# Kernel optimization log

Hardware: AMD Instinct MI355X
Metric: run time of the kernel (lower is better)

Reference implementation:

```python
import jax, jax.numpy as jnp
import numpy as np
import math

B, H, N, D = 4, 8, 2048, 64


def setup_inputs() -> dict:
    key = jax.random.key(0)
    kq, kk, kv = jax.random.split(key, 3)
    q = jax.random.normal(kq, (B, H, N, D), dtype=jnp.float32)
    k = jax.random.normal(kk, (B, H, N, D), dtype=jnp.float32)
    v = jax.random.normal(kv, (B, H, N, D), dtype=jnp.float32)
    return {"q": q, "k": k, "v": v}


def reference(q, k, v):
    # global_attention_Sub: expanded squared L2 distance ||q_i - k_j||^2
    # = qq_i - 2 q_i.k_j + kk_j, then softmax(-dist/sqrt(D)) @ v.
    scale = math.sqrt(q.shape[-1])
    inner = -2.0 * jnp.einsum('bhnd,bhmd->bhnm', q, k)          # [B,H,N,N]
    qq = jnp.sum(q * q, axis=-1, keepdims=True)                  # [B,H,N,1]
    kk = jnp.sum(k * k, axis=-1, keepdims=True)                  # [B,H,N,1]
    diff_sq = qq + inner + jnp.swapaxes(kk, -1, -2)              # [B,H,N,N]
    attn = jax.nn.softmax(-diff_sq / scale, axis=-1)
    x = jnp.einsum('bhnm,bhmd->bhnd', attn, v)                   # [B,H,N,D]
    return jnp.transpose(x, (0, 2, 1, 3))                        # [B,N,H,D]
```

## Files before the change

kernel.cpp:

```cpp
#include <hip/hip_runtime.h>

typedef __bf16 bf16x8 __attribute__((ext_vector_type(8)));
typedef float floatx4 __attribute__((ext_vector_type(4)));
typedef float floatx16 __attribute__((ext_vector_type(16)));
typedef unsigned int uintx4 __attribute__((ext_vector_type(4)));

constexpr int Bc = 4, Hc = 8, Nc = 2048, Dc = 64;
constexpr int BQ = 128;
constexpr int WQ = 32;
constexpr int TK = 64;
constexpr int NT = Nc / TK;
constexpr int NT2 = NT / 2;
constexpr float LOG2E = 1.44269504088896340736f;

constexpr size_t KSW_OFF = 0;
constexpr size_t VSW_OFF = (size_t)32 * NT * 8192;
constexpr size_t KKN_OFF = VSW_OFF * 2;

constexpr int SK_OFF  = 0;
constexpr int SV_OFF  = 32768;
constexpr int SKK_OFF = 65536;
constexpr int SL_OFF  = 66560;
constexpr int SMEM_BYTES = 67584;

typedef __attribute__((address_space(1))) const unsigned int gu32;
typedef __attribute__((address_space(3))) unsigned int lu32;
__device__ __forceinline__ void dma16(const void* g, void* l) {
    __builtin_amdgcn_global_load_lds((gu32*)g, (lu32*)l, 16, 0, 0);
}
__device__ __forceinline__ void dma4(const void* g, void* l) {
    __builtin_amdgcn_global_load_lds((gu32*)g, (lu32*)l, 4, 0, 0);
}

__device__ __forceinline__ unsigned pk2(float lo, float hi) {
    unsigned short a = __builtin_bit_cast(unsigned short, (__bf16)lo);
    unsigned short b = __builtin_bit_cast(unsigned short, (__bf16)hi);
    return (unsigned)a | ((unsigned)b << 16);
}

__global__ __launch_bounds__(256) void prep_kernel(
    const float* __restrict__ Kg, const float* __restrict__ Vg, char* __restrict__ ws)
{
    __shared__ float sT[64 * 68];
    const int tid = threadIdx.x;
    const int jt = blockIdx.x, bh = blockIdx.y;

    __bf16* Ksw = (__bf16*)(ws + KSW_OFF) + ((size_t)bh * NT + jt) * 4096;
    __bf16* Vsw = (__bf16*)(ws + VSW_OFF) + ((size_t)bh * NT + jt) * 4096;
    float*  kkn = (float*)(ws + KKN_OFF) + (size_t)bh * Nc + jt * 64;
    const size_t tb = ((size_t)bh * Nc + jt * 64) * Dc;

#pragma unroll
    for (int cc = 0; cc < 2; ++cc) {
        const int g   = tid + cc * 256;
        const int key = g >> 3, kcx = g & 7;
        const int kc  = kcx ^ (key & 7);
        const float* src = Kg + tb + key * 64 + kc * 8;
        float4 a = *(const float4*)src;
        float4 b = *(const float4*)(src + 4);
        float ss = a.x*a.x + a.y*a.y + a.z*a.z + a.w*a.w
                 + b.x*b.x + b.y*b.y + b.z*b.z + b.w*b.w;
        ss += __shfl_xor(ss, 1);
        ss += __shfl_xor(ss, 2);
        ss += __shfl_xor(ss, 4);
        if (kcx == 0) {
            const int k5 = key & 31, kt = key >> 5;
            const int rlo = k5 & 3, hh = (k5 >> 2) & 1, rhi = k5 >> 3;
            kkn[kt * 32 + hh * 16 + rhi * 4 + rlo] = -(ss * 0.125f * LOG2E);
        }
        bf16x8 c8;
        c8[0]=(__bf16)a.x; c8[1]=(__bf16)a.y; c8[2]=(__bf16)a.z; c8[3]=(__bf16)a.w;
        c8[4]=(__bf16)b.x; c8[5]=(__bf16)b.y; c8[6]=(__bf16)b.z; c8[7]=(__bf16)b.w;
        *(bf16x8*)(Ksw + g * 8) = c8;
    }
    {
        const int js = tid >> 2, dc = (tid & 3) * 16;
        const float* vr = Vg + tb + js * 64 + dc;
        float* dst = &sT[js * 68 + dc];
        *(float4*)dst       = *(const float4*)vr;
        *(float4*)(dst + 4) = *(const float4*)(vr + 4);
        *(float4*)(dst + 8) = *(const float4*)(vr + 8);
        *(float4*)(dst + 12)= *(const float4*)(vr + 12);
    }
    __syncthreads();
#pragma unroll
    for (int cc = 0; cc < 2; ++cc) {
        const int g = tid + cc * 256;
        const int d = g >> 3, kcx = g & 7;
        const int kc = kcx ^ (d & 7);
        bf16x8 c8;
#pragma unroll
        for (int e = 0; e < 8; ++e) {
            const int ee = (e + kcx) & 7;
            c8[ee] = (__bf16)sT[(kc * 8 + ee) * 68 + d];
        }
        *(bf16x8*)(Vsw + g * 8) = c8;
    }
}

__global__ __launch_bounds__(512, 4) void attn_kernel(
    const float* __restrict__ Qg, const char* __restrict__ ws, float* __restrict__ Og)
{
    __shared__ __align__(16) char smem[SMEM_BYTES];

    const int tid  = threadIdx.x;
    const int wave = tid >> 6;
    const int grp  = wave >> 2;
    const int sw   = wave & 3;
    const int lane = tid & 63;
    const int r31  = lane & 31;
    const int hi   = lane >> 5;

    const int lin  = blockIdx.x + (blockIdx.y << 4);
    const int xcd  = lin & 7, slot = lin >> 3;
    const int bh   = (xcd << 2) | (slot >> 4);
    const int qt   = slot & 15;

    const char* Kimg = ws + KSW_OFF + (size_t)bh * NT * 8192;
    const char* Vimg = ws + VSW_OFF + (size_t)bh * NT * 8192;
    const float* kkp = (const float*)(ws + KKN_OFF) + (size_t)bh * Nc;

    const float qscale = 0.25f * LOG2E;
    const int i0 = qt * BQ + sw * WQ;

    bf16x8 qf[4];
    {
        const float* qrow = Qg + ((size_t)bh * Nc + i0 + r31) * Dc + hi * 8;
#pragma unroll
        for (int ks = 0; ks < 4; ++ks) {
            float4 a = *(const float4*)(qrow + ks * 16);
            float4 b = *(const float4*)(qrow + ks * 16 + 4);
            bf16x8 f;
            f[0] = (__bf16)(a.x * qscale); f[1] = (__bf16)(a.y * qscale);
            f[2] = (__bf16)(a.z * qscale); f[3] = (__bf16)(a.w * qscale);
            f[4] = (__bf16)(b.x * qscale); f[5] = (__bf16)(b.y * qscale);
            f[6] = (__bf16)(b.z * qscale); f[7] = (__bf16)(b.w * qscale);
            qf[ks] = f;
        }
    }

    int off4[4];
#pragma unroll
    for (int ks = 0; ks < 4; ++ks)
        off4[ks] = r31 * 128 + (((ks * 2 + hi) ^ (r31 & 7)) << 4);

    floatx16 oacc[2];
#pragma unroll
    for (int dt = 0; dt < 2; ++dt)
#pragma unroll
        for (int e = 0; e < 16; ++e) oacc[dt][e] = 0.f;
    float lpr0 = 0.f, lpr1 = 0.f;

    auto stage = [&](int t, int nb) {
        const size_t tb = (size_t)t * 16384;
        const int off = tid * 16;
        dma16(Kimg + tb + off,        smem + SK_OFF + nb * 8192 + off);
        dma16(Kimg + tb + 8192 + off, smem + SK_OFF + 16384 + nb * 8192 + off);
        dma16(Vimg + tb + off,        smem + SV_OFF + nb * 8192 + off);
        dma16(Vimg + tb + 8192 + off, smem + SV_OFF + 16384 + nb * 8192 + off);
        if (tid < 128)
            dma4(kkp + t * 128 + tid, smem + SKK_OFF + nb * 512 + tid * 4);
    };

    stage(0, 0);

    for (int t = 0; t < NT2; ++t) {
        const int b = t & 1;
        __syncthreads();
        if (t + 1 < NT2) stage(t + 1, b ^ 1);

        const char* kb = smem + SK_OFF + grp * 16384 + b * 8192;
        const char* vb = smem + SV_OFF + grp * 16384 + b * 8192;
        const float* skkb = (const float*)(smem + SKK_OFF + b * 512) + grp * 64 + hi * 16;

        floatx16 st[2];
#pragma unroll
        for (int kt = 0; kt < 2; ++kt)
#pragma unroll
            for (int gi = 0; gi < 4; ++gi) {
                floatx4 kv = *(const floatx4*)(skkb + kt * 32 + gi * 4);
                st[kt][gi * 4 + 0] = kv[0]; st[kt][gi * 4 + 1] = kv[1];
                st[kt][gi * 4 + 2] = kv[2]; st[kt][gi * 4 + 3] = kv[3];
            }

        __builtin_amdgcn_s_setprio(1);
#pragma unroll
        for (int kt = 0; kt < 2; ++kt)
#pragma unroll
            for (int ks = 0; ks < 4; ++ks) {
                bf16x8 kf = *(const bf16x8*)(kb + kt * 4096 + off4[ks]);
                st[kt] = __builtin_amdgcn_mfma_f32_32x32x16_bf16(kf, qf[ks], st[kt], 0, 0, 0);
            }
        __builtin_amdgcn_s_setprio(0);

#pragma unroll
        for (int kt = 0; kt < 2; ++kt) {
            float p[16];
#pragma unroll
            for (int r = 0; r < 16; ++r) p[r] = __builtin_amdgcn_exp2f(st[kt][r]);
#pragma unroll
            for (int r = 0; r < 16; r += 2) { lpr0 += p[r]; lpr1 += p[r + 1]; }
            unsigned w[4][2];
#pragma unroll
            for (int g = 0; g < 4; ++g) {
                w[g][0] = pk2(p[4 * g + 0], p[4 * g + 1]);
                w[g][1] = pk2(p[4 * g + 2], p[4 * g + 3]);
            }
            __builtin_amdgcn_s_setprio(1);
#pragma unroll
            for (int sub = 0; sub < 2; ++sub) {
                unsigned a0 = w[2 * sub][0],     a1 = w[2 * sub][1];
                unsigned b0 = w[2 * sub + 1][0], b1 = w[2 * sub + 1][1];
                asm("v_permlane32_swap_b32 %0, %1" : "+v"(a0), "+v"(b0));
                asm("v_permlane32_swap_b32 %0, %1" : "+v"(a1), "+v"(b1));
                uintx4 u; u[0] = a0; u[1] = a1; u[2] = b0; u[3] = b1;
                bf16x8 pa = __builtin_bit_cast(bf16x8, u);
                const int ks = kt * 2 + sub;
#pragma unroll
                for (int dt = 0; dt < 2; ++dt) {
                    bf16x8 vf = *(const bf16x8*)(vb + dt * 4096 + off4[ks]);
                    oacc[dt] = __builtin_amdgcn_mfma_f32_32x32x16_bf16(pa, vf, oacc[dt], 0, 0, 0);
                }
            }
            __builtin_amdgcn_s_setprio(0);
        }
    }

    {
        float lpr = lpr0 + lpr1;
        float l = lpr + __shfl_xor(lpr, 32);
        if (!hi) *(float*)(smem + SL_OFF + (grp * 128 + sw * 32 + r31) * 4) = l;
    }
    __syncthreads();

    {
        char* slot = smem + wave * 4096;
        if (grp == 0) {
#pragma unroll
            for (int r = 0; r < 16; ++r)
                *(float*)(slot + r * 256 + lane * 4) = oacc[1][r];
        } else {
#pragma unroll
            for (int r = 0; r < 16; ++r)
                *(float*)(slot + r * 256 + lane * 4) = oacc[0][r];
        }
    }
    __syncthreads();

    floatx16 osum;
    if (grp == 0) osum = oacc[0]; else osum = oacc[1];
    {
        const char* pslot = smem + (wave ^ 4) * 4096;
#pragma unroll
        for (int r = 0; r < 16; ++r)
            osum[r] += *(const float*)(pslot + r * 256 + lane * 4);
    }

    const float* slp = (const float*)(smem + SL_OFF);
    const int b_ = bh >> 3, hh = bh & 7;
#pragma unroll
    for (int g = 0; g < 4; ++g) {
        floatx4 la = *(const floatx4*)(slp + sw * 32 + 8 * g + 4 * hi);
        floatx4 lb = *(const floatx4*)(slp + 128 + sw * 32 + 8 * g + 4 * hi);
#pragma unroll
        for (int rlo = 0; rlo < 4; ++rlo) {
            const float inv = 1.f / (la[rlo] + lb[rlo]);
            const int i = i0 + 8 * g + 4 * hi + rlo;
            float* orow = Og + (((size_t)b_ * Nc + i) * Hc + hh) * Dc + grp * 32 + r31;
            orow[0] = osum[4 * g + rlo] * inv;
        }
    }
}

extern "C" void kernel_launch(void* const* d_in, const int* in_sizes, int n_in,
                              void* d_out, int out_size, void* d_ws, size_t ws_size,
                              hipStream_t stream) {
    const float* q = (const float*)d_in[0];
    const float* k = (const float*)d_in[1];
    const float* v = (const float*)d_in[2];
    float* out = (float*)d_out;
    char* ws = (char*)d_ws;
    prep_kernel<<<dim3(NT, Bc * Hc), 256, 0, stream>>>(k, v, ws);
    attn_kernel<<<dim3(Nc / BQ, Bc * Hc), 512, 0, stream>>>(q, ws, out);
}
```

Measured before the change: 136.0 us.

## Software-pipeline QK^T of next tile with PV of previous tile

Restructures the main loop so each iteration issues the QK^T MFMAs for tile t together with the PV MFMAs for tile t-1, using softmax probabilities kept in registers from the previous iteration. The exp/pack softmax work then runs after the next stage's DMA is issued, so it can overlap with matrix work. A prologue and epilogue handle the first and last tiles. This adds a second __syncthreads per iteration and keeps more live registers for the pa fragments, which may hurt occupancy.

Result: no change. 138.5 us (+1.8%).

```diff
diff --git a/kernel.cpp b/kernel.cpp
--- a/kernel.cpp
+++ b/kernel.cpp
@@ -162,18 +162,8 @@
             dma4(kkp + t * 128 + tid, smem + SKK_OFF + nb * 512 + tid * 4);
     };
 
-    stage(0, 0);
-
-    for (int t = 0; t < NT2; ++t) {
-        const int b = t & 1;
-        __syncthreads();
-        if (t + 1 < NT2) stage(t + 1, b ^ 1);
-
-        const char* kb = smem + SK_OFF + grp * 16384 + b * 8192;
-        const char* vb = smem + SV_OFF + grp * 16384 + b * 8192;
+    auto kk_init = [&](int b, floatx16 st[2]) {
         const float* skkb = (const float*)(smem + SKK_OFF + b * 512) + grp * 64 + hi * 16;
-
-        floatx16 st[2];
 #pragma unroll
         for (int kt = 0; kt < 2; ++kt)
 #pragma unroll
@@ -182,17 +172,11 @@
                 st[kt][gi * 4 + 0] = kv[0]; st[kt][gi * 4 + 1] = kv[1];
                 st[kt][gi * 4 + 2] = kv[2]; st[kt][gi * 4 + 3] = kv[3];
             }
-
-        __builtin_amdgcn_s_setprio(1);
-#pragma unroll
-        for (int kt = 0; kt < 2; ++kt)
-#pragma unroll
-            for (int ks = 0; ks < 4; ++ks) {
-                bf16x8 kf = *(const bf16x8*)(kb + kt * 4096 + off4[ks]);
-                st[kt] = __builtin_amdgcn_mfma_f32_32x32x16_bf16(kf, qf[ks], st[kt], 0, 0, 0);
-            }
-        __builtin_amdgcn_s_setprio(0);
-
+    };
+
+    bf16x8 pa[2][2];
+
+    auto softmax = [&](floatx16 st[2]) {
 #pragma unroll
         for (int kt = 0; kt < 2; ++kt) {
             float p[16];
@@ -206,7 +190,6 @@
                 w[g][0] = pk2(p[4 * g + 0], p[4 * g + 1]);
                 w[g][1] = pk2(p[4 * g + 2], p[4 * g + 3]);
             }
-            __builtin_amdgcn_s_setprio(1);
 #pragma unroll
             for (int sub = 0; sub < 2; ++sub) {
                 unsigned a0 = w[2 * sub][0],     a1 = w[2 * sub][1];
@@ -214,16 +197,82 @@
                 asm("v_permlane32_swap_b32 %0, %1" : "+v"(a0), "+v"(b0));
                 asm("v_permlane32_swap_b32 %0, %1" : "+v"(a1), "+v"(b1));
                 uintx4 u; u[0] = a0; u[1] = a1; u[2] = b0; u[3] = b1;
-                bf16x8 pa = __builtin_bit_cast(bf16x8, u);
+                pa[kt][sub] = __builtin_bit_cast(bf16x8, u);
+            }
+        }
+    };
+
+    stage(0, 0);
+
+    {
+        __syncthreads();
+        stage(1, 1);
+        floatx16 st[2];
+        kk_init(0, st);
+        const char* kb = smem + SK_OFF + grp * 16384;
+        __builtin_amdgcn_s_setprio(1);
+#pragma unroll
+        for (int kt = 0; kt < 2; ++kt)
+#pragma unroll
+            for (int ks = 0; ks < 4; ++ks) {
+                bf16x8 kf = *(const bf16x8*)(kb + kt * 4096 + off4[ks]);
+                st[kt] = __builtin_amdgcn_mfma_f32_32x32x16_bf16(kf, qf[ks], st[kt], 0, 0, 0);
+            }
+        __builtin_amdgcn_s_setprio(0);
+        softmax(st);
+    }
+
+    for (int t = 1; t < NT2; ++t) {
+        const int b = t & 1;
+        __syncthreads();
+        const char* kb  = smem + SK_OFF + grp * 16384 + b * 8192;
+        const char* vbp = smem + SV_OFF + grp * 16384 + (b ^ 1) * 8192;
+
+        floatx16 st[2];
+        kk_init(b, st);
+
+        __builtin_amdgcn_s_setprio(1);
+#pragma unroll
+        for (int kt = 0; kt < 2; ++kt)
+#pragma unroll
+            for (int ks = 0; ks < 4; ++ks) {
+                bf16x8 kf = *(const bf16x8*)(kb + kt * 4096 + off4[ks]);
+                st[kt] = __builtin_amdgcn_mfma_f32_32x32x16_bf16(kf, qf[ks], st[kt], 0, 0, 0);
+            }
+#pragma unroll
+        for (int kt = 0; kt < 2; ++kt)
+#pragma unroll
+            for (int sub = 0; sub < 2; ++sub) {
                 const int ks = kt * 2 + sub;
 #pragma unroll
                 for (int dt = 0; dt < 2; ++dt) {
-                    bf16x8 vf = *(const bf16x8*)(vb + dt * 4096 + off4[ks]);
-                    oacc[dt] = __builtin_amdgcn_mfma_f32_32x32x16_bf16(pa, vf, oacc[dt], 0, 0, 0);
+                    bf16x8 vf = *(const bf16x8*)(vbp + dt * 4096 + off4[ks]);
+                    oacc[dt] = __builtin_amdgcn_mfma_f32_32x32x16_bf16(pa[kt][sub], vf, oacc[dt], 0, 0, 0);
                 }
             }
-            __builtin_amdgcn_s_setprio(0);
-        }
+        __builtin_amdgcn_s_setprio(0);
+
+        __syncthreads();
+        if (t + 1 < NT2) stage(t + 1, b ^ 1);
+
+        softmax(st);
+    }
+
+    {
+        const char* vbp = smem + SV_OFF + grp * 16384 + ((NT2 - 1) & 1) * 8192;
+        __builtin_amdgcn_s_setprio(1);
+#pragma unroll
+        for (int kt = 0; kt < 2; ++kt)
+#pragma unroll
+            for (int sub = 0; sub < 2; ++sub) {
+                const int ks = kt * 2 + sub;
+#pragma unroll
+                for (int dt = 0; dt < 2; ++dt) {
+                    bf16x8 vf = *(const bf16x8*)(vbp + dt * 4096 + off4[ks]);
+                    oacc[dt] = __builtin_amdgcn_mfma_f32_32x32x16_bf16(pa[kt][sub], vf, oacc[dt], 0, 0, 0);
+                }
+            }
+        __builtin_amdgcn_s_setprio(0);
     }
 
     {
```
